# Performance work log

Measured on AMD Instinct MI355X. Metric: run time of the kernel, lower is better.

The kernel has to match this reference:

```python
import jax, jax.numpy as jnp
import numpy as np

N = 20000      # nodes
E = 320000     # edges (before self loops)
IN = 128       # in_channels
HID = 64       # hid_channels
H = 4          # in_head
OUT = 16       # out_channels (classes)
SLOPE = 0.2    # GATv2 leaky_relu negative_slope default


def setup_inputs() -> dict:
    key = jax.random.key(0)
    ks = jax.random.split(key, 40)
    d = {}
    d["x"] = jax.random.normal(ks[0], (N, IN), jnp.float32)
    src = jax.random.randint(ks[1], (E,), 0, N)
    dst = jax.random.randint(ks[2], (E,), 0, N)
    d["edge_index"] = jnp.stack([src, dst]).astype(jnp.int32)
    # (in_ch, out_ch_per_head, heads) for the 4 GATv2Conv layers
    dims = [(IN, HID, H), (H * HID, HID, H), (H * HID, HID, H), (H * HID, OUT, 1)]
    ki = 3
    for li, (ic, oc, h) in enumerate(dims, 1):
        sc = 1.0 / np.sqrt(ic)
        d[f"w{li}l"] = jax.random.normal(ks[ki], (h * oc, ic), jnp.float32) * sc; ki += 1
        d[f"b{li}l"] = jnp.zeros((h * oc,), jnp.float32)
        d[f"w{li}r"] = jax.random.normal(ks[ki], (h * oc, ic), jnp.float32) * sc; ki += 1
        d[f"b{li}r"] = jnp.zeros((h * oc,), jnp.float32)
        d[f"a{li}"] = jax.random.normal(ks[ki], (h, oc), jnp.float32) * (1.0 / np.sqrt(oc)); ki += 1
        # output bias: [h*oc] if concat else [oc]; layer 4 is concat=False
        d[f"bo{li}"] = jnp.zeros((h * oc if li < 4 else oc,), jnp.float32)
    return d


def gatv2_layer(x, src, dst, wl, bl, wr, br, att, bias, heads, oc, concat):
    n = x.shape[0]
    xl = (x @ wl.T + bl).reshape(n, heads, oc)   # source transform
    xr = (x @ wr.T + br).reshape(n, heads, oc)   # target transform
    # per-edge GATv2 attention logit: a^T LeakyReLU(x_l[src] + x_r[dst])
    e = jax.nn.leaky_relu(xl[src] + xr[dst], SLOPE)          # [E,H,C]
    logits = jnp.einsum('ehc,hc->eh', e, att)                # [E,H]
    # segment softmax over incoming edges of each dst node
    m = jax.ops.segment_max(logits, dst, num_segments=n)     # [N,H]
    ex = jnp.exp(logits - m[dst])
    den = jax.ops.segment_sum(ex, dst, num_segments=n)
    alpha = ex / den[dst]                                    # [E,H]
    out = jax.ops.segment_sum(alpha[..., None] * xl[src], dst, num_segments=n)  # [N,H,C]
    out = out.reshape(n, heads * oc) if concat else out.mean(axis=1)
    return out + bias


def reference(x, edge_index,
              w1l, b1l, w1r, b1r, a1, bo1,
              w2l, b2l, w2r, b2r, a2, bo2,
              w3l, b3l, w3r, b3r, a3, bo3,
              w4l, b4l, w4r, b4r, a4, bo4):
    n = x.shape[0]
    loop = jnp.arange(n, dtype=edge_index.dtype)
    src = jnp.concatenate([edge_index[0], loop])  # PyG GATv2Conv adds self loops
    dst = jnp.concatenate([edge_index[1], loop])
    h = gatv2_layer(x, src, dst, w1l, b1l, w1r, b1r, a1, bo1, H, HID, True)
    h = jax.nn.relu(h)
    h = gatv2_layer(h, src, dst, w2l, b2l, w2r, b2r, a2, bo2, H, HID, True)
    h = jax.nn.relu(h)
    h = gatv2_layer(h, src, dst, w3l, b3l, w3r, b3r, a3, bo3, H, HID, True)
    h = jax.nn.relu(h)
    h = gatv2_layer(h, src, dst, w4l, b4l, w4r, b4r, a4, bo4, 1, OUT, False)
    return h
```

## Files before the change

kernel.cpp:

```cpp
#include <hip/hip_runtime.h>
#include <hip/hip_bf16.h>
#include <math.h>

#define NNODES 20000
#define NEDGES 320000
#define ETOT   (NEDGES + NNODES)
#define SLOPE  0.2f
#define MAXDEG 96

typedef __attribute__((ext_vector_type(8))) short bf16x8;
typedef __attribute__((ext_vector_type(4))) float f32x4;

__device__ inline unsigned short bfbits(float f) {
    __hip_bfloat16 h = __float2bfloat16(f);
    unsigned short u;
    __builtin_memcpy(&u, &h, 2);
    return u;
}
__device__ inline float bf2f(unsigned short u) {
    __hip_bfloat16 h;
    __builtin_memcpy(&h, &u, 2);
    return __bfloat162float(h);
}

__device__ inline void gload_lds16(const unsigned short* g, unsigned short* s) {
    __builtin_amdgcn_global_load_lds(
        (const __attribute__((address_space(1))) unsigned int*)g,
        (__attribute__((address_space(3))) unsigned int*)s, 16, 0, 0);
}

__global__ void slab_fill(const int* __restrict__ ei, int* __restrict__ fill,
                          int* __restrict__ slab) {
    int idx = blockIdx.x * blockDim.x + threadIdx.x;
    if (idx >= ETOT) return;
    int src, dst;
    if (idx < NEDGES) { src = ei[idx]; dst = ei[NEDGES + idx]; }
    else              { src = idx - NEDGES; dst = src; }
    int pos = atomicAdd(&fill[dst], 1);
    if (pos < MAXDEG) slab[dst * MAXDEG + pos] = src;
}

__global__ void convert_x(const float* __restrict__ x, unsigned short* __restrict__ Ap) {
    int idx = blockIdx.x * 256 + threadIdx.x;
    if (idx >= NNODES * 128) return;
    int m = idx >> 7, k = idx & 127;
    float f = x[idx];
    unsigned short hi = bfbits(f);
    unsigned short lo = bfbits(f - bf2f(hi));
    unsigned short* row = Ap + (size_t)m * 256;
    row[k] = hi; row[128 + k] = lo;
}

__global__ void convert_w(const float* __restrict__ w0, const float* __restrict__ w1,
                          unsigned short* __restrict__ Wp, int K, int n0, int ntot) {
    int idx = blockIdx.x * 256 + threadIdx.x;
    if (idx >= ntot * K) return;
    int n = idx / K, k = idx - n * K;
    float f = (n < n0) ? w0[n * K + k] : w1[(n - n0) * K + k];
    unsigned short hi = bfbits(f);
    unsigned short lo = bfbits(f - bf2f(hi));
    unsigned short* row = Wp + (size_t)n * 2 * K;
    row[k] = hi; row[K + k] = lo;
}

template <int NOUT>
__global__ __launch_bounds__(256) void gemm_mfma(
    const unsigned short* __restrict__ Ap, int KK,
    const unsigned short* __restrict__ Wp,
    const float* __restrict__ bias0, const float* __restrict__ bias1,
    float* __restrict__ O0, float* __restrict__ O1)
{
    __shared__ unsigned short AH[2 * 4096];
    __shared__ unsigned short AL[2 * 4096];
    __shared__ unsigned short BH[2 * 4096];
    __shared__ unsigned short BL[2 * 4096];

    int m0, nblk;
    if constexpr (NOUT == 512) {
        const int bid = blockIdx.x;
        const int xcd = bid & 7;
        const int k   = bid >> 3;
        nblk = k & 3;
        const int g = (k >> 2) * 8 + xcd;
        if (g >= (NNODES + 127) / 128) return;
        m0 = g * 128;
    } else {
        nblk = 0;
        m0 = blockIdx.x * 128;
    }
    const int n0 = nblk * 128;

    const int tid = threadIdx.x;
    const int l   = tid & 63;
    const int wid = tid >> 6;
    const int wr  = wid >> 1;
    const int wc  = wid & 1;

    const int srow = l & 15;
    const int skb  = l >> 4;
    const int W2K  = 2 * KK;

    int arow0 = m0 + wid * 16 + srow;
    int arow1 = arow0 + 64;
    arow0 = min(arow0, NNODES - 1);
    arow1 = min(arow1, NNODES - 1);
    const unsigned short* ahg0 = Ap + (size_t)arow0 * W2K + skb * 8;
    const unsigned short* ahg1 = Ap + (size_t)arow1 * W2K + skb * 8;
    int nrow0 = min(n0 + wid * 16 + srow, NOUT - 1);
    int nrow1 = min(n0 + wid * 16 + srow + 64, NOUT - 1);
    const unsigned short* bhg0 = Wp + (size_t)nrow0 * W2K + skb * 8;
    const unsigned short* bhg1 = Wp + (size_t)nrow1 * W2K + skb * 8;

    const int f0 = (0 * 4 + wid) * 512;
    const int f1 = (1 * 4 + wid) * 512;

    f32x4 acc[4][4];
    #pragma unroll
    for (int i = 0; i < 4; i++)
        #pragma unroll
        for (int j = 0; j < 4; j++)
            acc[i][j] = (f32x4){0.f, 0.f, 0.f, 0.f};

    const int S = KK >> 5;

    auto STAGE = [&](int buf, int k0) {
        const int bo = buf * 4096;
        gload_lds16(ahg0 + k0,      &AH[bo + f0]);
        gload_lds16(ahg1 + k0,      &AH[bo + f1]);
        gload_lds16(ahg0 + KK + k0, &AL[bo + f0]);
        gload_lds16(ahg1 + KK + k0, &AL[bo + f1]);
        gload_lds16(bhg0 + k0,      &BH[bo + f0]);
        gload_lds16(bhg1 + k0,      &BH[bo + f1]);
        gload_lds16(bhg0 + KK + k0, &BL[bo + f0]);
        gload_lds16(bhg1 + KK + k0, &BL[bo + f1]);
    };

    const int ra = (wr * 4) * 512 + l * 8;
    const int rb = (wc * 4) * 512 + l * 8;

    STAGE(0, 0);
    __syncthreads();

    int cur = 0;
    for (int s = 0; s < S; ++s) {
        if (s + 1 < S) STAGE(cur ^ 1, (s + 1) * 32);

        const int bo = cur * 4096;
        bf16x8 ah[4], al_[4], bh[4], bl[4];
        #pragma unroll
        for (int i = 0; i < 4; i++) {
            ah[i]  = *(const bf16x8*)&AH[bo + ra + i * 512];
            al_[i] = *(const bf16x8*)&AL[bo + ra + i * 512];
            bh[i]  = *(const bf16x8*)&BH[bo + rb + i * 512];
            bl[i]  = *(const bf16x8*)&BL[bo + rb + i * 512];
        }

        #pragma unroll
        for (int mi = 0; mi < 4; mi++)
            #pragma unroll
            for (int ni = 0; ni < 4; ni++) {
                acc[mi][ni] = __builtin_amdgcn_mfma_f32_16x16x32_bf16(ah[mi],  bh[ni], acc[mi][ni], 0, 0, 0);
                acc[mi][ni] = __builtin_amdgcn_mfma_f32_16x16x32_bf16(ah[mi],  bl[ni], acc[mi][ni], 0, 0, 0);
                acc[mi][ni] = __builtin_amdgcn_mfma_f32_16x16x32_bf16(al_[mi], bh[ni], acc[mi][ni], 0, 0, 0);
            }

        __syncthreads();
        cur ^= 1;
    }

    if constexpr (NOUT == 512) {
        const bool  left = (nblk < 2);
        float*       O   = left ? O0 : O1;
        const float* bs  = left ? bias0 : bias1;
        const int   cb   = (nblk & 1) * 128;
        #pragma unroll
        for (int mi = 0; mi < 4; mi++) {
            int r0 = m0 + wr * 64 + mi * 16 + (l >> 4) * 4;
            #pragma unroll
            for (int ni = 0; ni < 4; ni++) {
                int c = cb + wc * 64 + ni * 16 + (l & 15);
                float bv = bs[c];
                #pragma unroll
                for (int r = 0; r < 4; r++) {
                    int m = r0 + r;
                    if (m < NNODES) O[(size_t)m * 256 + c] = acc[mi][ni][r] + bv;
                }
            }
        }
    } else {
        #pragma unroll
        for (int mi = 0; mi < 4; mi++) {
            int r0 = m0 + wr * 64 + mi * 16 + (l >> 4) * 4;
            #pragma unroll
            for (int ni = 0; ni < 4; ni++) {
                int c = wc * 64 + ni * 16 + (l & 15);
                if (c >= 32) continue;
                float bv = (c < 16) ? bias0[c] : bias1[c - 16];
                #pragma unroll
                for (int r = 0; r < 4; r++) {
                    int m = r0 + r;
                    if (m < NNODES) O0[(size_t)m * 32 + c] = acc[mi][ni][r] + bv;
                }
            }
        }
    }
}

__device__ inline float edge_score(float4 v, float4 xrv, float4 attv) {
    float tx = v.x + xrv.x; tx = fmaxf(tx, SLOPE * tx);
    float ty = v.y + xrv.y; ty = fmaxf(ty, SLOPE * ty);
    float tz = v.z + xrv.z; tz = fmaxf(tz, SLOPE * tz);
    float tw = v.w + xrv.w; tw = fmaxf(tw, SLOPE * tw);
    float s = attv.x * tx + attv.y * ty + attv.z * tz + attv.w * tw;
    s += __shfl_xor(s, 1, 64);
    s += __shfl_xor(s, 2, 64);
    s += __shfl_xor(s, 4, 64);
    s += __shfl_xor(s, 8, 64);
    return s;
}

__device__ inline void sm_update(float s, float4 v, float& m, float& den, float4& acc) {
    float d = s - m;
    bool  r = d > 8.f;
    float e = __expf(r ? -d : d);
    float sc = r ? e : 1.f;
    float pw = r ? 1.f : e;
    m = r ? s : m;
    den = den * sc + pw;
    acc.x = acc.x * sc + pw * v.x;
    acc.y = acc.y * sc + pw * v.y;
    acc.z = acc.z * sc + pw * v.z;
    acc.w = acc.w * sc + pw * v.w;
}

__device__ inline void sm_merge(float& m0, float& den0, float4& acc0,
                                float m1, float den1, float4 acc1) {
    float nm = fmaxf(m0, m1);
    float sa = __expf(m0 - nm);
    float sb = __expf(m1 - nm);
    den0 = den0 * sa + den1 * sb;
    acc0.x = acc0.x * sa + acc1.x * sb;
    acc0.y = acc0.y * sa + acc1.y * sb;
    acc0.z = acc0.z * sa + acc1.z * sb;
    acc0.w = acc0.w * sa + acc1.w * sb;
    m0 = nm;
}

__global__ __launch_bounds__(128) void gat_attn_node(
    const float* __restrict__ xl, const float* __restrict__ xr,
    const float* __restrict__ att, const float* __restrict__ bo,
    const int* __restrict__ fill, const int* __restrict__ slab,
    unsigned short* __restrict__ outp)
{
    const int lane = threadIdx.x & 63;
    const int node = blockIdx.x * 2 + (threadIdx.x >> 6);
    if (node >= NNODES) return;

    const unsigned laneoff = (unsigned)lane << 4;
    const char*    xlb     = (const char*)xl;

    const float4 attv = *(const float4*)&att[lane * 4];
    const float4 xrv  = *(const float4*)((const char*)xr + ((unsigned)node << 10) + laneoff);
    const float4 bov  = *(const float4*)&bo[lane * 4];

    const int  deg = min(fill[node], MAXDEG);
    const int* sl  = slab + node * MAXDEG;

    float  m0 = -1e30f, m1 = -1e30f, m2 = -1e30f, m3 = -1e30f;
    float  d0 = 0.f, d1 = 0.f, d2 = 0.f, d3 = 0.f;
    float4 a0 = make_float4(0.f, 0.f, 0.f, 0.f);
    float4 a1 = a0, a2 = a0, a3 = a0;

    auto gather = [&](int src) -> float4 {
        return *(const float4*)(xlb + (((unsigned)src << 10) + laneoff));
    };

    auto batch = [&](float4 v0, float4 v1, float4 v2, float4 v3) {
        float s0 = edge_score(v0, xrv, attv);
        float s1 = edge_score(v1, xrv, attv);
        float s2 = edge_score(v2, xrv, attv);
        float s3 = edge_score(v3, xrv, attv);
        bool need = (s0 - m0 > 8.f) | (s1 - m1 > 8.f) | (s2 - m2 > 8.f) | (s3 - m3 > 8.f);
        if (!__any(need)) {
            float p0 = __expf(s0 - m0);
            float p1 = __expf(s1 - m1);
            float p2 = __expf(s2 - m2);
            float p3 = __expf(s3 - m3);
            d0 += p0; d1 += p1; d2 += p2; d3 += p3;
            a0.x += p0 * v0.x; a0.y += p0 * v0.y; a0.z += p0 * v0.z; a0.w += p0 * v0.w;
            a1.x += p1 * v1.x; a1.y += p1 * v1.y; a1.z += p1 * v1.z; a1.w += p1 * v1.w;
            a2.x += p2 * v2.x; a2.y += p2 * v2.y; a2.z += p2 * v2.z; a2.w += p2 * v2.w;
            a3.x += p3 * v3.x; a3.y += p3 * v3.y; a3.z += p3 * v3.z; a3.w += p3 * v3.w;
        } else {
            sm_update(s0, v0, m0, d0, a0);
            sm_update(s1, v1, m1, d1, a1);
            sm_update(s2, v2, m2, d2, a2);
            sm_update(s3, v3, m3, d3, a3);
        }
    };

    float4 v0, v1, v2, v3;
    int p = 0;
    if (deg >= 4) {
        int4 s4 = *(const int4*)sl;
        v0 = gather(s4.x); v1 = gather(s4.y);
        v2 = gather(s4.z); v3 = gather(s4.w);
        p = 4;
    }
    for (; p + 4 <= deg; p += 4) {
        int4 s4 = *(const int4*)&sl[p];
        float4 w0 = gather(s4.x);
        float4 w1 = gather(s4.y);
        float4 w2 = gather(s4.z);
        float4 w3 = gather(s4.w);
        batch(v0, v1, v2, v3);
        v0 = w0; v1 = w1; v2 = w2; v3 = w3;
    }
    if (deg >= 4) batch(v0, v1, v2, v3);
    for (; p < deg; ++p) {
        float4 v = gather(sl[p]);
        float s = edge_score(v, xrv, attv);
        sm_update(s, v, m0, d0, a0);
    }

    sm_merge(m0, d0, a0, m1, d1, a1);
    sm_merge(m2, d2, a2, m3, d3, a3);
    sm_merge(m0, d0, a0, m2, d2, a2);

    float4 o;
    o.x = fmaxf(a0.x / d0 + bov.x, 0.f);
    o.y = fmaxf(a0.y / d0 + bov.y, 0.f);
    o.z = fmaxf(a0.z / d0 + bov.z, 0.f);
    o.w = fmaxf(a0.w / d0 + bov.w, 0.f);

    unsigned short* row = outp + (size_t)node * 512 + lane * 4;
    ushort4 hv, lv;
    hv.x = bfbits(o.x); hv.y = bfbits(o.y); hv.z = bfbits(o.z); hv.w = bfbits(o.w);
    lv.x = bfbits(o.x - bf2f(hv.x));
    lv.y = bfbits(o.y - bf2f(hv.y));
    lv.z = bfbits(o.z - bf2f(hv.z));
    lv.w = bfbits(o.w - bf2f(hv.w));
    *(ushort4*)(row)       = hv;
    *(ushort4*)(row + 256) = lv;
}

__global__ __launch_bounds__(128) void gat_attn_final(
    const float* __restrict__ O32,
    const float* __restrict__ att, const float* __restrict__ bo,
    const int* __restrict__ fill, const int* __restrict__ slab,
    float* __restrict__ out)
{
    const int lane = threadIdx.x & 63;
    const int sub  = lane >> 4;
    const int c    = lane & 15;

    const int node = (blockIdx.x * 2 + (threadIdx.x >> 6)) * 4 + sub;
    if (node >= NNODES) return;

    const unsigned coff = (unsigned)c << 2;
    const char*    ob   = (const char*)O32;

    const float attc = att[c];
    const float xrc  = *(const float*)(ob + (((unsigned)node << 7) + 64 + coff));

    const int  deg = min(fill[node], MAXDEG);
    const int* sl  = slab + node * MAXDEG;

    float m0 = -1e30f, m1 = -1e30f, d0 = 0.f, d1 = 0.f, a0 = 0.f, a1 = 0.f;

    int p = 0;
    for (; p + 2 <= deg; p += 2) {
        int srcA = sl[p];
        int srcB = sl[p + 1];
        float vA = *(const float*)(ob + (((unsigned)srcA << 7) + coff));
        float vB = *(const float*)(ob + (((unsigned)srcB << 7) + coff));
        float tA = vA + xrc; tA = fmaxf(tA, SLOPE * tA);
        float tB = vB + xrc; tB = fmaxf(tB, SLOPE * tB);
        float sA = attc * tA;
        float sB = attc * tB;
        sA += __shfl_xor(sA, 1, 64);  sB += __shfl_xor(sB, 1, 64);
        sA += __shfl_xor(sA, 2, 64);  sB += __shfl_xor(sB, 2, 64);
        sA += __shfl_xor(sA, 4, 64);  sB += __shfl_xor(sB, 4, 64);
        sA += __shfl_xor(sA, 8, 64);  sB += __shfl_xor(sB, 8, 64);
        {
            float dd = sA - m0; bool r = dd > 8.f;
            float e = __expf(r ? -dd : dd);
            float sc = r ? e : 1.f, pw = r ? 1.f : e;
            m0 = r ? sA : m0;
            d0 = d0 * sc + pw;
            a0 = a0 * sc + pw * vA;
        }
        {
            float dd = sB - m1; bool r = dd > 8.f;
            float e = __expf(r ? -dd : dd);
            float sc = r ? e : 1.f, pw = r ? 1.f : e;
            m1 = r ? sB : m1;
            d1 = d1 * sc + pw;
            a1 = a1 * sc + pw * vB;
        }
    }
    if (p < deg) {
        int src = sl[p];
        float v = *(const float*)(ob + (((unsigned)src << 7) + coff));
        float t = v + xrc; t = fmaxf(t, SLOPE * t);
        float s = attc * t;
        s += __shfl_xor(s, 1, 64);
        s += __shfl_xor(s, 2, 64);
        s += __shfl_xor(s, 4, 64);
        s += __shfl_xor(s, 8, 64);
        float dd = s - m0; bool r = dd > 8.f;
        float e = __expf(r ? -dd : dd);
        float sc = r ? e : 1.f, pw = r ? 1.f : e;
        m0 = r ? s : m0;
        d0 = d0 * sc + pw;
        a0 = a0 * sc + pw * v;
    }

    float nm = fmaxf(m0, m1);
    float sa = __expf(m0 - nm);
    float sb = __expf(m1 - nm);
    float den = d0 * sa + d1 * sb;
    out[(size_t)node * 16 + c] = (a0 * sa + a1 * sb) / den + bo[c];
}

extern "C" void kernel_launch(void* const* d_in, const int* in_sizes, int n_in,
                              void* d_out, int out_size, void* d_ws, size_t ws_size,
                              hipStream_t stream)
{
    const float* x   = (const float*)d_in[0];
    const int*   ei  = (const int*)d_in[1];
    const float* w1l = (const float*)d_in[2];  const float* b1l = (const float*)d_in[3];
    const float* w1r = (const float*)d_in[4];  const float* b1r = (const float*)d_in[5];
    const float* a1  = (const float*)d_in[6];  const float* bo1 = (const float*)d_in[7];
    const float* w2l = (const float*)d_in[8];  const float* b2l = (const float*)d_in[9];
    const float* w2r = (const float*)d_in[10]; const float* b2r = (const float*)d_in[11];
    const float* a2  = (const float*)d_in[12]; const float* bo2 = (const float*)d_in[13];
    const float* w3l = (const float*)d_in[14]; const float* b3l = (const float*)d_in[15];
    const float* w3r = (const float*)d_in[16]; const float* b3r = (const float*)d_in[17];
    const float* a3  = (const float*)d_in[18]; const float* bo3 = (const float*)d_in[19];
    const float* w4l = (const float*)d_in[20]; const float* b4l = (const float*)d_in[21];
    const float* w4r = (const float*)d_in[22]; const float* b4r = (const float*)d_in[23];
    const float* a4  = (const float*)d_in[24]; const float* bo4 = (const float*)d_in[25];

    char* ws = (char*)d_ws;
    auto carve = [&](size_t bytes) {
        void* p = ws;
        ws += (bytes + 255) & ~(size_t)255;
        return p;
    };
    unsigned short* Ap = (unsigned short*)carve((size_t)NNODES * 512 * sizeof(unsigned short));
    float* xl = (float*)carve((size_t)NNODES * 256 * sizeof(float));
    float* xr = (float*)carve((size_t)NNODES * 256 * sizeof(float));
    float* O32 = xl;
    unsigned short* Wp1 = (unsigned short*)carve((size_t)512 * 256 * sizeof(unsigned short));
    unsigned short* Wp2 = (unsigned short*)carve((size_t)512 * 512 * sizeof(unsigned short));
    unsigned short* Wp3 = (unsigned short*)carve((size_t)512 * 512 * sizeof(unsigned short));
    unsigned short* Wp4 = (unsigned short*)carve((size_t)32 * 512 * sizeof(unsigned short));
    int* fill = (int*)carve((size_t)NNODES * sizeof(int));
    int* slab = (int*)carve((size_t)NNODES * MAXDEG * sizeof(int));

    const int eblocks = (ETOT + 255) / 256;

    convert_x<<<(NNODES * 128 + 255) / 256, 256, 0, stream>>>(x, Ap);
    convert_w<<<(512 * 128 + 255) / 256, 256, 0, stream>>>(w1l, w1r, Wp1, 128, 256, 512);
    convert_w<<<(512 * 256 + 255) / 256, 256, 0, stream>>>(w2l, w2r, Wp2, 256, 256, 512);
    convert_w<<<(512 * 256 + 255) / 256, 256, 0, stream>>>(w3l, w3r, Wp3, 256, 256, 512);
    convert_w<<<(32 * 256 + 255) / 256, 256, 0, stream>>>(w4l, w4r, Wp4, 256, 16, 32);

    hipMemsetAsync(fill, 0, (size_t)NNODES * sizeof(int), stream);
    slab_fill<<<eblocks, 256, 0, stream>>>(ei, fill, slab);

    const int g512 = 640;
    const int ablocks = (NNODES + 1) / 2;

    gemm_mfma<512><<<g512, 256, 0, stream>>>(Ap, 128, Wp1, b1l, b1r, xl, xr);
    gat_attn_node<<<ablocks, 128, 0, stream>>>(xl, xr, a1, bo1, fill, slab, Ap);

    gemm_mfma<512><<<g512, 256, 0, stream>>>(Ap, 256, Wp2, b2l, b2r, xl, xr);
    gat_attn_node<<<ablocks, 128, 0, stream>>>(xl, xr, a2, bo2, fill, slab, Ap);

    gemm_mfma<512><<<g512, 256, 0, stream>>>(Ap, 256, Wp3, b3l, b3r, xl, xr);
    gat_attn_node<<<ablocks, 128, 0, stream>>>(xl, xr, a3, bo3, fill, slab, Ap);

    gemm_mfma<32><<<(NNODES + 127) / 128, 256, 0, stream>>>(Ap, 256, Wp4, b4l, b4r, O32, O32);
    gat_attn_final<<<(NNODES + 7) / 8, 128, 0, stream>>>(O32, a4, bo4, fill, slab, (float*)d_out);
}
```

Baseline: 327.2 us.

## Split attention per head with head-major layout, degree-sorted nodes, XCD-aware mapping

The GEMM epilogue now writes xl/xr in head-major layout [head][node][64]. The attention kernel handles four nodes per wavefront for a single head, with 16 lanes per node, and reads a node order sorted by degree so nodes sharing a wave have similar degree. Blocks are mapped so that each head's gather data stays within a fixed pair of XCDs, which should improve L2 locality for the random source gathers. The change adds binning kernels and masked padding work for uneven degrees inside a wave. It also relies on the assumption that blocks are dispatched round-robin across XCDs.

```diff
diff --git a/kernel.cpp b/kernel.cpp
--- a/kernel.cpp
+++ b/kernel.cpp
@@ -38,6 +38,25 @@
     else              { src = idx - NEDGES; dst = src; }
     int pos = atomicAdd(&fill[dst], 1);
     if (pos < MAXDEG) slab[dst * MAXDEG + pos] = src;
+}
+
+__global__ void bin_count(const int* __restrict__ fill, int* __restrict__ bcnt) {
+    int n = blockIdx.x * 256 + threadIdx.x;
+    if (n >= NNODES) return;
+    atomicAdd(&bcnt[min(fill[n], 31)], 1);
+}
+__global__ void bin_scan(const int* __restrict__ bcnt, int* __restrict__ bfill) {
+    if (threadIdx.x == 0) {
+        int run = 0;
+        for (int i = 0; i < 32; i++) { bfill[i] = run; run += bcnt[i]; }
+    }
+}
+__global__ void bin_fill(const int* __restrict__ fill, int* __restrict__ bfill,
+                         int* __restrict__ order) {
+    int n = blockIdx.x * 256 + threadIdx.x;
+    if (n >= NNODES) return;
+    int pos = atomicAdd(&bfill[min(fill[n], 31)], 1);
+    order[pos] = n;
 }
 
 __global__ void convert_x(const float* __restrict__ x, unsigned short* __restrict__ Ap) {
@@ -179,11 +198,13 @@
             #pragma unroll
             for (int ni = 0; ni < 4; ni++) {
                 int c = cb + wc * 64 + ni * 16 + (l & 15);
+                int head = c >> 6, ch = c & 63;
                 float bv = bs[c];
                 #pragma unroll
                 for (int r = 0; r < 4; r++) {
                     int m = r0 + r;
-                    if (m < NNODES) O[(size_t)m * 256 + c] = acc[mi][ni][r] + bv;
+                    if (m < NNODES)
+                        O[((size_t)head * NNODES + m) * 64 + ch] = acc[mi][ni][r] + bv;
                 }
             }
         }
@@ -219,12 +240,13 @@
     return s;
 }
 
-__device__ inline void sm_update(float s, float4 v, float& m, float& den, float4& acc) {
+__device__ inline void sm_upd(float s, float4 v, bool act,
+                              float& m, float& den, float4& acc) {
     float d = s - m;
-    bool  r = d > 8.f;
+    bool  r = act && (d > 8.f);
     float e = __expf(r ? -d : d);
     float sc = r ? e : 1.f;
-    float pw = r ? 1.f : e;
+    float pw = act ? (r ? 1.f : e) : 0.f;
     m = r ? s : m;
     den = den * sc + pw;
     acc.x = acc.x * sc + pw * v.x;
@@ -246,25 +268,37 @@
     m0 = nm;
 }
 
-__global__ __launch_bounds__(128) void gat_attn_node(
+__global__ __launch_bounds__(64) void gat_attn_head(
     const float* __restrict__ xl, const float* __restrict__ xr,
     const float* __restrict__ att, const float* __restrict__ bo,
     const int* __restrict__ fill, const int* __restrict__ slab,
+    const int* __restrict__ order,
     unsigned short* __restrict__ outp)
 {
-    const int lane = threadIdx.x & 63;
-    const int node = blockIdx.x * 2 + (threadIdx.x >> 6);
-    if (node >= NNODES) return;
-
-    const unsigned laneoff = (unsigned)lane << 4;
-    const char*    xlb     = (const char*)xl;
-
-    const float4 attv = *(const float4*)&att[lane * 4];
-    const float4 xrv  = *(const float4*)((const char*)xr + ((unsigned)node << 10) + laneoff);
-    const float4 bov  = *(const float4*)&bo[lane * 4];
+    const int b    = blockIdx.x;
+    const int xcd  = b & 7;
+    const int head = xcd >> 1;
+    const int grp  = (b >> 3) * 2 + (xcd & 1);
+    const int lane = threadIdx.x;
+    const int sub  = lane >> 4;
+    const int c    = lane & 15;
+
+    const int node = order[grp * 4 + sub];
+    const unsigned coff = (unsigned)c << 4;
+
+    const char* xlh = (const char*)xl + (size_t)head * (NNODES * 256);
+    const char* xrh = (const char*)xr + (size_t)head * (NNODES * 256);
+
+    const float4 attv = *(const float4*)&att[head * 64 + c * 4];
+    const float4 xrv  = *(const float4*)(xrh + ((unsigned)node << 8) + coff);
+    const float4 bov  = *(const float4*)&bo[head * 64 + c * 4];
 
     const int  deg = min(fill[node], MAXDEG);
     const int* sl  = slab + node * MAXDEG;
+
+    int maxd = deg;
+    maxd = max(maxd, __shfl_xor(maxd, 16, 64));
+    maxd = max(maxd, __shfl_xor(maxd, 32, 64));
 
     float  m0 = -1e30f, m1 = -1e30f, m2 = -1e30f, m3 = -1e30f;
     float  d0 = 0.f, d1 = 0.f, d2 = 0.f, d3 = 0.f;
@@ -272,56 +306,53 @@
     float4 a1 = a0, a2 = a0, a3 = a0;
 
     auto gather = [&](int src) -> float4 {
-        return *(const float4*)(xlb + (((unsigned)src << 10) + laneoff));
+        return *(const float4*)(xlh + (((unsigned)src << 8) + coff));
     };
 
-    auto batch = [&](float4 v0, float4 v1, float4 v2, float4 v3) {
+    auto batch = [&](float4 v0, float4 v1, float4 v2, float4 v3, int pb) {
+        const bool A0 = pb + 0 < deg, A1 = pb + 1 < deg;
+        const bool A2 = pb + 2 < deg, A3 = pb + 3 < deg;
         float s0 = edge_score(v0, xrv, attv);
         float s1 = edge_score(v1, xrv, attv);
         float s2 = edge_score(v2, xrv, attv);
         float s3 = edge_score(v3, xrv, attv);
-        bool need = (s0 - m0 > 8.f) | (s1 - m1 > 8.f) | (s2 - m2 > 8.f) | (s3 - m3 > 8.f);
+        bool need = (A0 & (s0 - m0 > 8.f)) | (A1 & (s1 - m1 > 8.f)) |
+                    (A2 & (s2 - m2 > 8.f)) | (A3 & (s3 - m3 > 8.f));
         if (!__any(need)) {
-            float p0 = __expf(s0 - m0);
-            float p1 = __expf(s1 - m1);
-            float p2 = __expf(s2 - m2);
-            float p3 = __expf(s3 - m3);
+            float p0 = A0 ? __expf(s0 - m0) : 0.f;
+            float p1 = A1 ? __expf(s1 - m1) : 0.f;
+            float p2 = A2 ? __expf(s2 - m2) : 0.f;
+            float p3 = A3 ? __expf(s3 - m3) : 0.f;
             d0 += p0; d1 += p1; d2 += p2; d3 += p3;
             a0.x += p0 * v0.x; a0.y += p0 * v0.y; a0.z += p0 * v0.z; a0.w += p0 * v0.w;
             a1.x += p1 * v1.x; a1.y += p1 * v1.y; a1.z += p1 * v1.z; a1.w += p1 * v1.w;
             a2.x += p2 * v2.x; a2.y += p2 * v2.y; a2.z += p2 * v2.z; a2.w += p2 * v2.w;
             a3.x += p3 * v3.x; a3.y += p3 * v3.y; a3.z += p3 * v3.z; a3.w += p3 * v3.w;
         } else {
-            sm_update(s0, v0, m0, d0, a0);
-            sm_update(s1, v1, m1, d1, a1);
-            sm_update(s2, v2, m2, d2, a2);
-            sm_update(s3, v3, m3, d3, a3);
+            sm_upd(s0, v0, A0, m0, d0, a0);
+            sm_upd(s1, v1, A1, m1, d1, a1);
+            sm_upd(s2, v2, A2, m2, d2, a2);
+            sm_upd(s3, v3, A3, m3, d3, a3);
         }
     };
 
-    float4 v0, v1, v2, v3;
-    int p = 0;
-    if (deg >= 4) {
-        int4 s4 = *(const int4*)sl;
-        v0 = gather(s4.x); v1 = gather(s4.y);
-        v2 = gather(s4.z); v3 = gather(s4.w);
-        p = 4;
-    }
-    for (; p + 4 <= deg; p += 4) {
-        int4 s4 = *(const int4*)&sl[p];
-        float4 w0 = gather(s4.x);
-        float4 w1 = gather(s4.y);
-        float4 w2 = gather(s4.z);
-        float4 w3 = gather(s4.w);
-        batch(v0, v1, v2, v3);
+    int4 s4 = *(const int4*)sl;
+    float4 v0 = gather((0 < deg) ? s4.x : node);
+    float4 v1 = gather((1 < deg) ? s4.y : node);
+    float4 v2 = gather((2 < deg) ? s4.z : node);
+    float4 v3 = gather((3 < deg) ? s4.w : node);
+    int pc = 0;
+    for (int p = 4; p < maxd; p += 4) {
+        int4 t4 = *(const int4*)&sl[p];
+        float4 w0 = gather((p + 0 < deg) ? t4.x : node);
+        float4 w1 = gather((p + 1 < deg) ? t4.y : node);
+        float4 w2 = gather((p + 2 < deg) ? t4.z : node);
+        float4 w3 = gather((p + 3 < deg) ? t4.w : node);
+        batch(v0, v1, v2, v3, pc);
         v0 = w0; v1 = w1; v2 = w2; v3 = w3;
-    }
-    if (deg >= 4) batch(v0, v1, v2, v3);
-    for (; p < deg; ++p) {
-        float4 v = gather(sl[p]);
-        float s = edge_score(v, xrv, attv);
-        sm_update(s, v, m0, d0, a0);
-    }
+        pc = p;
+    }
+    batch(v0, v1, v2, v3, pc);
 
     sm_merge(m0, d0, a0, m1, d1, a1);
     sm_merge(m2, d2, a2, m3, d3, a3);
@@ -333,7 +364,7 @@
     o.z = fmaxf(a0.z / d0 + bov.z, 0.f);
     o.w = fmaxf(a0.w / d0 + bov.w, 0.f);
 
-    unsigned short* row = outp + (size_t)node * 512 + lane * 4;
+    unsigned short* row = outp + (size_t)node * 512 + head * 64 + c * 4;
     ushort4 hv, lv;
     hv.x = bfbits(o.x); hv.y = bfbits(o.y); hv.z = bfbits(o.z); hv.w = bfbits(o.w);
     lv.x = bfbits(o.x - bf2f(hv.x));
@@ -456,10 +487,14 @@
     unsigned short* Wp2 = (unsigned short*)carve((size_t)512 * 512 * sizeof(unsigned short));
     unsigned short* Wp3 = (unsigned short*)carve((size_t)512 * 512 * sizeof(unsigned short));
     unsigned short* Wp4 = (unsigned short*)carve((size_t)32 * 512 * sizeof(unsigned short));
-    int* fill = (int*)carve((size_t)NNODES * sizeof(int));
-    int* slab = (int*)carve((size_t)NNODES * MAXDEG * sizeof(int));
+    int* fill  = (int*)carve((size_t)NNODES * sizeof(int));
+    int* slab  = (int*)carve((size_t)NNODES * MAXDEG * sizeof(int));
+    int* bcnt  = (int*)carve(32 * sizeof(int));
+    int* bfill = (int*)carve(32 * sizeof(int));
+    int* order = (int*)carve((size_t)NNODES * sizeof(int));
 
     const int eblocks = (ETOT + 255) / 256;
+    const int nblocks = (NNODES + 255) / 256;
 
     convert_x<<<(NNODES * 128 + 255) / 256, 256, 0, stream>>>(x, Ap);
     convert_w<<<(512 * 128 + 255) / 256, 256, 0, stream>>>(w1l, w1r, Wp1, 128, 256, 512);
@@ -468,19 +503,23 @@
     convert_w<<<(32 * 256 + 255) / 256, 256, 0, stream>>>(w4l, w4r, Wp4, 256, 16, 32);
 
     hipMemsetAsync(fill, 0, (size_t)NNODES * sizeof(int), stream);
+    hipMemsetAsync(bcnt, 0, 32 * sizeof(int), stream);
     slab_fill<<<eblocks, 256, 0, stream>>>(ei, fill, slab);
+    bin_count<<<nblocks, 256, 0, stream>>>(fill, bcnt);
+    bin_scan<<<1, 64, 0, stream>>>(bcnt, bfill);
+    bin_fill<<<nblocks, 256, 0, stream>>>(fill, bfill, order);
 
     const int g512 = 640;
-    const int ablocks = (NNODES + 1) / 2;
+    const int ah   = 20000;
 
     gemm_mfma<512><<<g512, 256, 0, stream>>>(Ap, 128, Wp1, b1l, b1r, xl, xr);
-    gat_attn_node<<<ablocks, 128, 0, stream>>>(xl, xr, a1, bo1, fill, slab, Ap);
+    gat_attn_head<<<ah, 64, 0, stream>>>(xl, xr, a1, bo1, fill, slab, order, Ap);
 
     gemm_mfma<512><<<g512, 256, 0, stream>>>(Ap, 256, Wp2, b2l, b2r, xl, xr);
-    gat_attn_node<<<ablocks, 128, 0, stream>>>(xl, xr, a2, bo2, fill, slab, Ap);
+    gat_attn_head<<<ah, 64, 0, stream>>>(xl, xr, a2, bo2, fill, slab, order, Ap);
 
     gemm_mfma<512><<<g512, 256, 0, stream>>>(Ap, 256, Wp3, b3l, b3r, xl, xr);
-    gat_attn_node<<<ablocks, 128, 0, stream>>>(xl, xr, a3, bo3, fill, slab, Ap);
+    gat_attn_head<<<ah, 64, 0, stream>>>(xl, xr, a3, bo3, fill, slab, order, Ap);
 
     gemm_mfma<32><<<(NNODES + 127) / 128, 256, 0, stream>>>(Ap, 256, Wp4, b4l, b4r, O32, O32);
     gat_attn_final<<<(NNODES + 7) / 8, 128, 0, stream>>>(O32, a4, bo4, fill, slab, (float*)d_out);
```

Result: slower. 410.9 us (+25.6%).
